# Kernel tuning notes

Measured on AMD Instinct MI355X. Metric: run time of the kernel, lower is better.

Reference implementation:

```python
import jax, jax.numpy as jnp
import numpy as np

# SE3 transform stored as [..., 7] = [quat(wxyz), translation(xyz)]

def qmul(a, b):
    w1, x1, y1, z1 = a[..., 0], a[..., 1], a[..., 2], a[..., 3]
    w2, x2, y2, z2 = b[..., 0], b[..., 1], b[..., 2], b[..., 3]
    return jnp.stack([
        w1 * w2 - x1 * x2 - y1 * y2 - z1 * z2,
        w1 * x2 + x1 * w2 + y1 * z2 - z1 * y2,
        w1 * y2 - x1 * z2 + y1 * w2 + z1 * x2,
        w1 * z2 + x1 * y2 - y1 * x2 + z1 * w2,
    ], axis=-1)


def qrot(q, v):
    # rotate vectors v [...,3] by unit quaternions q [...,4] (wxyz)
    qv, w = q[..., 1:], q[..., 0:1]
    t = 2.0 * jnp.cross(qv, v)
    return v + w * t + jnp.cross(qv, t)


def se3_mul(Ta, Tb):
    qa, ta = Ta[..., :4], Ta[..., 4:]
    qb, tb = Tb[..., :4], Tb[..., 4:]
    return jnp.concatenate([qmul(qa, qb), qrot(qa, tb) + ta], axis=-1)


def se3_inv(T):
    q, t = T[..., :4], T[..., 4:]
    qi = q * jnp.array([1.0, -1.0, -1.0, -1.0], dtype=q.dtype)
    return jnp.concatenate([qi, -qrot(qi, t)], axis=-1)


def _rand_se3(key, n):
    kq, kt = jax.random.split(key)
    q = jax.random.normal(kq, (n, 4), dtype=jnp.float32)
    q = q / jnp.linalg.norm(q, axis=-1, keepdims=True)
    t = jax.random.normal(kt, (n, 3), dtype=jnp.float32)
    return jnp.concatenate([q, t], axis=-1)


def setup_inputs() -> dict:
    E, B = 500000, 64
    node_dim = edge_dim = global_dim = hidden_dim = 128
    DIM = 7
    in_dim = 2 * node_dim + DIM + edge_dim + global_dim  # 519
    key = jax.random.key(0)
    ks = jax.random.split(key, 12)
    return {
        "xfeati": jax.random.normal(ks[0], (E, node_dim), dtype=jnp.float32),
        "xfeatj": jax.random.normal(ks[1], (E, node_dim), dtype=jnp.float32),
        "edge_feat": jax.random.normal(ks[2], (E, edge_dim), dtype=jnp.float32),
        "Ti": _rand_se3(ks[3], E),
        "Tj": _rand_se3(ks[4], E),
        "Tij_hat": _rand_se3(ks[5], E),
        "u": jax.random.normal(ks[6], (B, global_dim), dtype=jnp.float32),
        "batch": jax.random.randint(ks[7], (E,), 0, B, dtype=jnp.int32),
        "W1": jax.random.normal(ks[8], (in_dim, hidden_dim), dtype=jnp.float32) / np.sqrt(in_dim),
        "b1": jnp.zeros((hidden_dim,), dtype=jnp.float32),
        "W2": jax.random.normal(ks[9], (hidden_dim, edge_dim), dtype=jnp.float32) / np.sqrt(hidden_dim),
        "b2": jnp.zeros((edge_dim,), dtype=jnp.float32),
    }


def reference(xfeati, xfeatj, edge_feat, Ti, Tj, Tij_hat, u, batch, W1, b1, W2, b2):
    Tij = se3_mul(Tj, se3_inv(Ti))         # [E, 7]
    T_err = se3_mul(Tij_hat, se3_inv(Tij))  # [E, 7] -> .vec()
    feat_cat = jnp.concatenate([xfeati, xfeatj, edge_feat, T_err, u[batch]], axis=1)
    h = jax.nn.relu(feat_cat @ W1 + b1)
    edge_feat_out = edge_feat + (h @ W2 + b2)
    return (edge_feat_out, Tij_hat)
```

## Files before the change

### kernel.cpp

```cpp
#include <hip/hip_runtime.h>

typedef __attribute__((ext_vector_type(4))) float f32x4;
typedef __attribute__((ext_vector_type(8))) short bf16x8;

__device__ __forceinline__ unsigned short f2bf(float f){
  unsigned int x = __float_as_uint(f);
  return (unsigned short)((x + 0x7fffu + ((x >> 16) & 1u)) >> 16);
}

__device__ __forceinline__ unsigned int cvt2(float lo, float hi){
  unsigned int r;
  asm("v_cvt_pk_bf16_f32 %0, %1, %2" : "=v"(r) : "v"(lo), "v"(hi));
  return r;
}

struct Q  { float w,x,y,z; };
struct V3 { float x,y,z; };
struct M3 { float m[9]; };

__device__ __forceinline__ Q qmul(Q a, Q b){
  return { a.w*b.w - a.x*b.x - a.y*b.y - a.z*b.z,
           a.w*b.x + a.x*b.w + a.y*b.z - a.z*b.y,
           a.w*b.y - a.x*b.z + a.y*b.w + a.z*b.x,
           a.w*b.z + a.x*b.y - a.y*b.x + a.z*b.w };
}
__device__ __forceinline__ Q qconj(Q q){ return { q.w, -q.x, -q.y, -q.z }; }
__device__ __forceinline__ M3 q2R(Q q){
  const float w=q.w, x=q.x, y=q.y, z=q.z;
  M3 R;
  R.m[0]=1.f-2.f*(y*y+z*z); R.m[1]=2.f*(x*y-w*z);     R.m[2]=2.f*(x*z+w*y);
  R.m[3]=2.f*(x*y+w*z);     R.m[4]=1.f-2.f*(x*x+z*z); R.m[5]=2.f*(y*z-w*x);
  R.m[6]=2.f*(x*z-w*y);     R.m[7]=2.f*(y*z+w*x);     R.m[8]=1.f-2.f*(x*x+y*y);
  return R;
}
__device__ __forceinline__ V3 mv (M3 R, V3 v){
  return { R.m[0]*v.x + R.m[1]*v.y + R.m[2]*v.z,
           R.m[3]*v.x + R.m[4]*v.y + R.m[5]*v.z,
           R.m[6]*v.x + R.m[7]*v.y + R.m[8]*v.z };
}
__device__ __forceinline__ V3 mtv(M3 R, V3 v){
  return { R.m[0]*v.x + R.m[3]*v.y + R.m[6]*v.z,
           R.m[1]*v.x + R.m[4]*v.y + R.m[7]*v.z,
           R.m[2]*v.x + R.m[5]*v.y + R.m[8]*v.z };
}

__global__ void prep_kernel(const float* __restrict__ W1, const float* __restrict__ W2,
                            unsigned short* __restrict__ W1p, unsigned short* __restrict__ W2p){
  const int N1 = 128*544;
  int gid = blockIdx.x*256 + threadIdx.x;
  if (gid < N1){
    int c = gid / 544, k = gid % 544;
    W1p[gid] = (k < 519) ? f2bf(W1[(size_t)k*128 + c]) : (unsigned short)0;
  } else if (gid < N1 + 128*128){
    int g = gid - N1;
    int c = g >> 7, k = g & 127;
    W2p[g] = f2bf(W2[(size_t)k*128 + c]);
  }
}

template<bool WSP>
__global__ __launch_bounds__(512) void edge_k(
    const float* __restrict__ xfi, const float* __restrict__ xfj, const float* __restrict__ ef,
    const float* __restrict__ Ti,  const float* __restrict__ Tj,  const float* __restrict__ Th,
    const int*   __restrict__ batch, const float* __restrict__ u,
    const float* __restrict__ W1,  const float* __restrict__ b1,
    const float* __restrict__ W2,  const float* __restrict__ b2,
    const unsigned short* __restrict__ W1p, const unsigned short* __restrict__ W2p,
    float* __restrict__ outE, float* __restrict__ outT, int E)
{
  __shared__ __align__(16) unsigned short tailb[64][168];
  __shared__ __align__(16) unsigned short fbuf[64][136];
  __shared__ __align__(16) unsigned short hbf[64][136];
  __shared__ float tib[448], tjb[448], thb[448];
  __shared__ int ibat_s[64];

  const int tid = threadIdx.x;
  const long base = (long)blockIdx.x * 64;

  {
    const long flatBase = base * 7;
    const long flatMax  = (long)E * 7;
    if (tid < 448){
      long fi = flatBase + tid; if (fi >= flatMax) fi = flatMax - 1;
      const float vi = Ti[fi], vj = Tj[fi], vh = Th[fi];
      tib[tid] = vi; tjb[tid] = vj; thb[tid] = vh;
      if (flatBase + tid < flatMax) outT[flatBase + tid] = vh;
    }
  }
  __syncthreads();

  if (tid < 64){
    const long row = base + tid;
    const long rc  = row < E ? row : (long)(E-1);
    const float* pi = &tib[tid*7];
    const float* pj = &tjb[tid*7];
    const float* ph = &thb[tid*7];
    Q  qi{pi[0],pi[1],pi[2],pi[3]};  V3 tti{pi[4],pi[5],pi[6]};
    Q  qj{pj[0],pj[1],pj[2],pj[3]};  V3 ttj{pj[4],pj[5],pj[6]};
    Q  qh{ph[0],ph[1],ph[2],ph[3]};  V3 tth{ph[4],ph[5],ph[6]};
    M3 Ri = q2R(qi), Rj = q2R(qj), Rh = q2R(qh);
    V3 a  = mtv(Rj, ttj);
    V3 bv = mv(Ri, a);
    V3 c  { tti.x - bv.x, tti.y - bv.y, tti.z - bv.z };
    V3 d  = mv(Rh, c);
    Q  qe = qmul(qmul(qh, qi), qconj(qj));
    tailb[tid][0] = f2bf(qe.w);
    tailb[tid][1] = f2bf(qe.x);
    tailb[tid][2] = f2bf(qe.y);
    tailb[tid][3] = f2bf(qe.z);
    tailb[tid][4] = f2bf(tth.x + d.x);
    tailb[tid][5] = f2bf(tth.y + d.y);
    tailb[tid][6] = f2bf(tth.z + d.z);
    ibat_s[tid] = batch[rc];
  }
  __syncthreads();

  for (int idx = tid; idx < 64*128; idx += 512){
    const int e = idx >> 7, c = idx & 127;
    tailb[e][7 + c] = f2bf(u[(size_t)ibat_s[e]*128 + c]);
  }
  for (int idx = tid; idx < 64*33; idx += 512){
    const int e = idx / 33, c = idx % 33;
    tailb[e][135 + c] = 0;
  }

  const int lane = tid & 63, wv = tid >> 6;
  const int l15 = lane & 15, l4 = lane >> 4;
  const int col = wv*16 + l15;

  f32x4 acc1[4];
  {
    const float bv = b1[col];
    #pragma unroll
    for (int a = 0; a < 4; ++a){
      #pragma unroll
      for (int r = 0; r < 4; ++r) acc1[a][r] = bv;
    }
  }

  const float* fps[3] = { xfi, xfj, ef };
  for (int fb = 0; fb < 3; ++fb){
    const float* F = fps[fb];
    __syncthreads();
    #pragma unroll
    for (int i = 0; i < 4; ++i){
      const int idx = i*512 + tid;
      const int e = idx >> 5, c4 = (idx & 31) << 2;
      long rr = base + e; if (rr >= E) rr = E-1;
      const float4 v = *reinterpret_cast<const float4*>(F + (size_t)rr*128 + c4);
      unsigned int* dst = reinterpret_cast<unsigned int*>(&fbuf[e][c4]);
      dst[0] = cvt2(v.x, v.y);
      dst[1] = cvt2(v.z, v.w);
    }
    __syncthreads();
    #pragma unroll
    for (int kc = 0; kc < 4; ++kc){
      const int kl = kc*32 + l4*8;
      bf16x8 afr[4];
      #pragma unroll
      for (int a = 0; a < 4; ++a)
        afr[a] = *reinterpret_cast<const bf16x8*>(&fbuf[a*16 + l15][kl]);
      bf16x8 Bv;
      if (WSP){
        Bv = *reinterpret_cast<const bf16x8*>(W1p + (size_t)col*544 + fb*128 + kl);
      } else {
        float w[8];
        #pragma unroll
        for (int j = 0; j < 8; ++j)
          w[j] = W1[(size_t)(fb*128 + kl + j)*128 + col];
        union { bf16x8 v; unsigned int ui[4]; } B;
        B.ui[0] = cvt2(w[0], w[1]);
        B.ui[1] = cvt2(w[2], w[3]);
        B.ui[2] = cvt2(w[4], w[5]);
        B.ui[3] = cvt2(w[6], w[7]);
        Bv = B.v;
      }
      #pragma unroll
      for (int a = 0; a < 4; ++a)
        acc1[a] = __builtin_amdgcn_mfma_f32_16x16x32_bf16(afr[a], Bv, acc1[a], 0, 0, 0);
    }
  }
  #pragma unroll
  for (int tc = 0; tc < 5; ++tc){
    const int kt = tc*32 + l4*8;
    bf16x8 afr[4];
    #pragma unroll
    for (int a = 0; a < 4; ++a)
      afr[a] = *reinterpret_cast<const bf16x8*>(&tailb[a*16 + l15][kt]);
    bf16x8 Bv;
    if (WSP){
      Bv = *reinterpret_cast<const bf16x8*>(W1p + (size_t)col*544 + 384 + kt);
    } else {
      float w[8];
      #pragma unroll
      for (int j = 0; j < 8; ++j){
        const int kk = 384 + kt + j;
        w[j] = (kk < 519) ? W1[(size_t)kk*128 + col] : 0.f;
      }
      union { bf16x8 v; unsigned int ui[4]; } B;
      B.ui[0] = cvt2(w[0], w[1]);
      B.ui[1] = cvt2(w[2], w[3]);
      B.ui[2] = cvt2(w[4], w[5]);
      B.ui[3] = cvt2(w[6], w[7]);
      Bv = B.v;
    }
    #pragma unroll
    for (int a = 0; a < 4; ++a)
      acc1[a] = __builtin_amdgcn_mfma_f32_16x16x32_bf16(afr[a], Bv, acc1[a], 0, 0, 0);
  }

  #pragma unroll
  for (int a = 0; a < 4; ++a){
    #pragma unroll
    for (int r = 0; r < 4; ++r)
      hbf[a*16 + l4*4 + r][col] = f2bf(fmaxf(acc1[a][r], 0.f));
  }
  __syncthreads();

  f32x4 acc2[4];
  {
    const float bv2 = b2[col];
    #pragma unroll
    for (int a = 0; a < 4; ++a){
      #pragma unroll
      for (int r = 0; r < 4; ++r){
        long orow = base + a*16 + l4*4 + r;
        if (orow >= E) orow = E-1;
        acc2[a][r] = ef[(size_t)orow*128 + col] + bv2;
      }
    }
  }
  #pragma unroll
  for (int ks = 0; ks < 4; ++ks){
    const int k0 = ks*32 + l4*8;
    bf16x8 afr[4];
    #pragma unroll
    for (int a = 0; a < 4; ++a)
      afr[a] = *reinterpret_cast<const bf16x8*>(&hbf[a*16 + l15][k0]);
    bf16x8 Bv;
    if (WSP){
      Bv = *reinterpret_cast<const bf16x8*>(W2p + (size_t)col*128 + k0);
    } else {
      float w[8];
      #pragma unroll
      for (int j = 0; j < 8; ++j)
        w[j] = W2[(size_t)(k0 + j)*128 + col];
      union { bf16x8 v; unsigned int ui[4]; } B;
      B.ui[0] = cvt2(w[0], w[1]);
      B.ui[1] = cvt2(w[2], w[3]);
      B.ui[2] = cvt2(w[4], w[5]);
      B.ui[3] = cvt2(w[6], w[7]);
      Bv = B.v;
    }
    #pragma unroll
    for (int a = 0; a < 4; ++a)
      acc2[a] = __builtin_amdgcn_mfma_f32_16x16x32_bf16(afr[a], Bv, acc2[a], 0, 0, 0);
  }

  #pragma unroll
  for (int a = 0; a < 4; ++a){
    #pragma unroll
    for (int r = 0; r < 4; ++r){
      const long orow = base + a*16 + l4*4 + r;
      if (orow < E) outE[(size_t)orow*128 + col] = acc2[a][r];
    }
  }
}

extern "C" void kernel_launch(void* const* d_in, const int* in_sizes, int n_in,
                              void* d_out, int out_size, void* d_ws, size_t ws_size,
                              hipStream_t stream){
  const float* xfi  = (const float*)d_in[0];
  const float* xfj  = (const float*)d_in[1];
  const float* ef   = (const float*)d_in[2];
  const float* Ti   = (const float*)d_in[3];
  const float* Tj   = (const float*)d_in[4];
  const float* Th   = (const float*)d_in[5];
  const float* u    = (const float*)d_in[6];
  const int*   bat  = (const int*)d_in[7];
  const float* W1   = (const float*)d_in[8];
  const float* b1   = (const float*)d_in[9];
  const float* W2   = (const float*)d_in[10];
  const float* b2   = (const float*)d_in[11];
  const int E = in_sizes[0] / 128;

  float* outE = (float*)d_out;
  float* outT = outE + (size_t)E * 128;

  const int grid = (E + 63) / 64;
  const size_t need = (size_t)(128*544 + 128*128) * sizeof(unsigned short);
  if (d_ws != nullptr && ws_size >= need){
    unsigned short* W1p = (unsigned short*)d_ws;
    unsigned short* W2p = W1p + (size_t)128*544;
    prep_kernel<<<(128*544 + 128*128 + 255)/256, 256, 0, stream>>>(W1, W2, W1p, W2p);
    edge_k<true><<<grid, 512, 0, stream>>>(xfi, xfj, ef, Ti, Tj, Th, bat, u,
                                           W1, b1, W2, b2, W1p, W2p, outE, outT, E);
  } else {
    edge_k<false><<<grid, 512, 0, stream>>>(xfi, xfj, ef, Ti, Tj, Th, bat, u,
                                            W1, b1, W2, b2, nullptr, nullptr, outE, outT, E);
  }
}
```

Measured before the change: 283.2 us.

## Prefetch first feature tile early, drop batch-index barrier, raise MFMA wave priority

Moves the load and bf16 conversion of the xfeati tile to the start of the kernel, so it overlaps with the SE3 pose loads and the quaternion math. The first GEMM chunk is peeled out of the feature loop to consume it. Removes the shared batch-index array and one barrier by reading batch directly inside the u-gather loop, at the cost of redundant global reads of batch. Wraps the MFMA sections in s_setprio so waves in the compute phase get issue priority over waves that are loading.

```diff
diff --git a/kernel.cpp b/kernel.cpp
--- a/kernel.cpp
+++ b/kernel.cpp
@@ -72,10 +72,20 @@
   __shared__ __align__(16) unsigned short fbuf[64][136];
   __shared__ __align__(16) unsigned short hbf[64][136];
   __shared__ float tib[448], tjb[448], thb[448];
-  __shared__ int ibat_s[64];
 
   const int tid = threadIdx.x;
   const long base = (long)blockIdx.x * 64;
+
+  #pragma unroll
+  for (int i = 0; i < 4; ++i){
+    const int idx = i*512 + tid;
+    const int e = idx >> 5, c4 = (idx & 31) << 2;
+    long rr = base + e; if (rr >= E) rr = E-1;
+    const float4 v = *reinterpret_cast<const float4*>(xfi + (size_t)rr*128 + c4);
+    unsigned int* dst = reinterpret_cast<unsigned int*>(&fbuf[e][c4]);
+    dst[0] = cvt2(v.x, v.y);
+    dst[1] = cvt2(v.z, v.w);
+  }
 
   {
     const long flatBase = base * 7;
@@ -90,8 +100,6 @@
   __syncthreads();
 
   if (tid < 64){
-    const long row = base + tid;
-    const long rc  = row < E ? row : (long)(E-1);
     const float* pi = &tib[tid*7];
     const float* pj = &tjb[tid*7];
     const float* ph = &thb[tid*7];
@@ -111,13 +119,11 @@
     tailb[tid][4] = f2bf(tth.x + d.x);
     tailb[tid][5] = f2bf(tth.y + d.y);
     tailb[tid][6] = f2bf(tth.z + d.z);
-    ibat_s[tid] = batch[rc];
-  }
-  __syncthreads();
-
+  }
   for (int idx = tid; idx < 64*128; idx += 512){
     const int e = idx >> 7, c = idx & 127;
-    tailb[e][7 + c] = f2bf(u[(size_t)ibat_s[e]*128 + c]);
+    long rc = base + e; if (rc >= E) rc = E-1;
+    tailb[e][7 + c] = f2bf(u[(size_t)batch[rc]*128 + c]);
   }
   for (int idx = tid; idx < 64*33; idx += 512){
     const int e = idx / 33, c = idx % 33;
@@ -138,8 +144,37 @@
     }
   }
 
+  __builtin_amdgcn_s_setprio(1);
+  #pragma unroll
+  for (int kc = 0; kc < 4; ++kc){
+    const int kl = kc*32 + l4*8;
+    bf16x8 afr[4];
+    #pragma unroll
+    for (int a = 0; a < 4; ++a)
+      afr[a] = *reinterpret_cast<const bf16x8*>(&fbuf[a*16 + l15][kl]);
+    bf16x8 Bv;
+    if (WSP){
+      Bv = *reinterpret_cast<const bf16x8*>(W1p + (size_t)col*544 + kl);
+    } else {
+      float w[8];
+      #pragma unroll
+      for (int j = 0; j < 8; ++j)
+        w[j] = W1[(size_t)(kl + j)*128 + col];
+      union { bf16x8 v; unsigned int ui[4]; } B;
+      B.ui[0] = cvt2(w[0], w[1]);
+      B.ui[1] = cvt2(w[2], w[3]);
+      B.ui[2] = cvt2(w[4], w[5]);
+      B.ui[3] = cvt2(w[6], w[7]);
+      Bv = B.v;
+    }
+    #pragma unroll
+    for (int a = 0; a < 4; ++a)
+      acc1[a] = __builtin_amdgcn_mfma_f32_16x16x32_bf16(afr[a], Bv, acc1[a], 0, 0, 0);
+  }
+  __builtin_amdgcn_s_setprio(0);
+
   const float* fps[3] = { xfi, xfj, ef };
-  for (int fb = 0; fb < 3; ++fb){
+  for (int fb = 1; fb < 3; ++fb){
     const float* F = fps[fb];
     __syncthreads();
     #pragma unroll
@@ -153,6 +188,7 @@
       dst[1] = cvt2(v.z, v.w);
     }
     __syncthreads();
+    __builtin_amdgcn_s_setprio(1);
     #pragma unroll
     for (int kc = 0; kc < 4; ++kc){
       const int kl = kc*32 + l4*8;
@@ -179,7 +215,10 @@
       for (int a = 0; a < 4; ++a)
         acc1[a] = __builtin_amdgcn_mfma_f32_16x16x32_bf16(afr[a], Bv, acc1[a], 0, 0, 0);
     }
-  }
+    __builtin_amdgcn_s_setprio(0);
+  }
+
+  __builtin_amdgcn_s_setprio(1);
   #pragma unroll
   for (int tc = 0; tc < 5; ++tc){
     const int kt = tc*32 + l4*8;
@@ -208,6 +247,7 @@
     for (int a = 0; a < 4; ++a)
       acc1[a] = __builtin_amdgcn_mfma_f32_16x16x32_bf16(afr[a], Bv, acc1[a], 0, 0, 0);
   }
+  __builtin_amdgcn_s_setprio(0);
 
   #pragma unroll
   for (int a = 0; a < 4; ++a){
@@ -230,6 +270,7 @@
       }
     }
   }
+  __builtin_amdgcn_s_setprio(1);
   #pragma unroll
   for (int ks = 0; ks < 4; ++ks){
     const int k0 = ks*32 + l4*8;
@@ -256,6 +297,7 @@
     for (int a = 0; a < 4; ++a)
       acc2[a] = __builtin_amdgcn_mfma_f32_16x16x32_bf16(afr[a], Bv, acc2[a], 0, 0, 0);
   }
+  __builtin_amdgcn_s_setprio(0);
 
   #pragma unroll
   for (int a = 0; a < 4; ++a){
```

Result: slower. 295.2 us (+4.3%).
